# Performance work log

Measured on AMD Instinct MI355X. Metric: run time of the kernel, lower is better.

The kernel has to match this reference:

```python
import jax, jax.numpy as jnp
import numpy as np

N = 100000
E = 3200000
F_IN = 128
H = 64


def _glorot(key, fan_in, fan_out):
    lim = jnp.sqrt(6.0 / (fan_in + fan_out))
    return jax.random.uniform(key, (fan_in, fan_out), minval=-lim, maxval=lim, dtype=jnp.float32)


def setup_inputs() -> dict:
    key = jax.random.key(0)
    ks = jax.random.split(key, 16)
    x = jax.random.normal(ks[0], (N, F_IN), dtype=jnp.float32)
    edge_index = jax.random.randint(ks[1], (2, E), 0, N, dtype=jnp.int32)
    batch = jnp.zeros((N,), dtype=jnp.int32)
    dims = [(F_IN, H), (H, H // 2), (H // 2, H // 4), (H // 4, H // 2), (H // 2, H), (H, F_IN)]
    params = {}
    for i, (fi, fo) in enumerate(dims):
        params[f"W{i+1}"] = _glorot(ks[2 + i], fi, fo)
        params[f"b{i+1}"] = jnp.zeros((fo,), dtype=jnp.float32)
    params["Wf"] = _glorot(ks[10], F_IN, F_IN)
    params["bf"] = jnp.zeros((F_IN,), dtype=jnp.float32)
    return {"x": x, "edge_index": edge_index, "batch": batch, **params}


def _gcn_norm(edge_index, num_nodes):
    # PyG GCNConv: add self-loops, sym-normalize with deg^{-1/2}
    loop = jnp.arange(num_nodes, dtype=edge_index.dtype)
    row = jnp.concatenate([edge_index[0], loop])  # source j
    col = jnp.concatenate([edge_index[1], loop])  # target i
    deg = jax.ops.segment_sum(jnp.ones_like(col, dtype=jnp.float32), col, num_segments=num_nodes)
    dinv = jnp.where(deg > 0, jax.lax.rsqrt(deg), 0.0)
    norm = dinv[row] * dinv[col]
    return row, col, norm


def _gcn_conv(h, W, b, row, col, norm, num_nodes):
    h = h @ W  # linear first (no bias in lin), then normalized scatter-add
    msg = h[row] * norm[:, None]
    agg = jax.ops.segment_sum(msg, col, num_segments=num_nodes)
    return agg + b


def reference(x, edge_index, batch, W1, b1, W2, b2, W3, b3, W4, b4, W5, b5, W6, b6, Wf, bf):
    n = x.shape[0]
    row, col, norm = _gcn_norm(edge_index, n)
    h = jax.nn.relu(_gcn_conv(x, W1, b1, row, col, norm, n))
    h = jax.nn.relu(_gcn_conv(h, W2, b2, row, col, norm, n))
    h = jax.nn.relu(_gcn_conv(h, W3, b3, row, col, norm, n))
    h = jax.nn.relu(_gcn_conv(h, W4, b4, row, col, norm, n))
    h = jax.nn.relu(_gcn_conv(h, W5, b5, row, col, norm, n))
    h = jax.nn.relu(_gcn_conv(h, W6, b6, row, col, norm, n))
    return h @ Wf + bf
```

## Files before the change

### kernel.cpp

```cpp
#include <hip/hip_runtime.h>
#include <hip/hip_fp16.h>

#define BLK 256
#define NBSHIFT 9
#define MAXNB 200
#define GPART 512

typedef _Float16 half4v __attribute__((ext_vector_type(4)));
typedef _Float16 half8v __attribute__((ext_vector_type(8)));
typedef float    f32x4v __attribute__((ext_vector_type(4)));

__device__ __forceinline__ float4 ld4(const float* p) { return *(const float4*)p; }

__global__ __launch_bounds__(BLK) void p1_hist_k(const int* __restrict__ cols, int* __restrict__ hist,
                                                 int E, int nb) {
    __shared__ int h[MAXNB];
    const int tid = threadIdx.x, g = blockIdx.x;
    for (int b = tid; b < nb; b += BLK) h[b] = 0;
    __syncthreads();
    const int chunk = (E + GPART - 1) / GPART;
    const int start = g * chunk, end = min(E, start + chunk);
    for (int e = start + tid; e < end; e += BLK) atomicAdd(&h[cols[e] >> NBSHIFT], 1);
    __syncthreads();
    for (int b = tid; b < nb; b += BLK) hist[b * GPART + g] = h[b];
}
__global__ __launch_bounds__(256) void p2a_k(const int* __restrict__ hist, int* __restrict__ bstart,
                                             int nb, int E) {
    __shared__ int s[256];
    const int t = threadIdx.x;
    int tot = 0;
    if (t < nb) {
        const int* hp = &hist[t * GPART];
        for (int g = 0; g < GPART; g++) tot += hp[g];
    }
    s[t] = tot;
    __syncthreads();
    for (int o = 1; o < 256; o <<= 1) {
        int v = s[t] + ((t >= o) ? s[t - o] : 0);
        __syncthreads();
        s[t] = v;
        __syncthreads();
    }
    if (t < nb) bstart[t] = s[t] - tot;
    if (t == 0) bstart[nb] = E;
}
__global__ __launch_bounds__(256) void p2b_k(int* __restrict__ hist, const int* __restrict__ bstart) {
    __shared__ int s[GPART];
    const int b = blockIdx.x, t = threadIdx.x;
    const int v0 = hist[b * GPART + t], v1 = hist[b * GPART + 256 + t];
    s[t] = v0; s[256 + t] = v1;
    __syncthreads();
    for (int o = 1; o < GPART; o <<= 1) {
        const int a0 = s[t] + ((t >= o) ? s[t - o] : 0);
        const int a1 = s[256 + t] + ((256 + t >= o) ? s[256 + t - o] : 0);
        __syncthreads();
        s[t] = a0; s[256 + t] = a1;
        __syncthreads();
    }
    const int base = bstart[b];
    hist[b * GPART + t] = base + s[t] - v0;
    hist[b * GPART + 256 + t] = base + s[256 + t] - v1;
}
__global__ __launch_bounds__(BLK) void p3_part_k(const int* __restrict__ rows, const int* __restrict__ cols,
                                                 const int* __restrict__ hist, int2* __restrict__ pairs,
                                                 int E, int nb) {
    __shared__ int tail[MAXNB];
    const int tid = threadIdx.x, g = blockIdx.x;
    for (int b = tid; b < nb; b += BLK) tail[b] = hist[b * GPART + g];
    __syncthreads();
    const int chunk = (E + GPART - 1) / GPART;
    const int start = g * chunk, end = min(E, start + chunk);
    for (int e = start + tid; e < end; e += BLK) {
        const int r = rows[e], c = cols[e];
        const int pos = atomicAdd(&tail[c >> NBSHIFT], 1);
        pairs[pos] = make_int2(r, c);
    }
}
__global__ __launch_bounds__(BLK) void p4_fill_k(const int2* __restrict__ pairs, const int* __restrict__ bstart,
                                                 int* __restrict__ P, float* __restrict__ dinv,
                                                 int* __restrict__ srow, int n) {
    __shared__ int dh[1 << NBSHIFT];
    __shared__ int tl[1 << NBSHIFT];
    const int b = blockIdx.x, t = threadIdx.x;
    const int base = b << NBSHIFT;
    const int nnod = min(1 << NBSHIFT, n - base);
    const int lo = bstart[b], hi = bstart[b + 1];
    dh[t] = 0; dh[256 + t] = 0;
    __syncthreads();
    for (int e = lo + t; e < hi; e += BLK) atomicAdd(&dh[pairs[e].y - base], 1);
    __syncthreads();
    const int v0 = dh[t], v1 = dh[256 + t];
    tl[t] = v0; tl[256 + t] = v1;
    __syncthreads();
    for (int o = 1; o < (1 << NBSHIFT); o <<= 1) {
        const int a0 = tl[t] + ((t >= o) ? tl[t - o] : 0);
        const int a1 = tl[256 + t] + ((256 + t >= o) ? tl[256 + t - o] : 0);
        __syncthreads();
        tl[t] = a0; tl[256 + t] = a1;
        __syncthreads();
    }
    const int s0 = lo + tl[t] - v0;
    const int s1 = lo + tl[256 + t] - v1;
    __syncthreads();
    tl[t] = s0; tl[256 + t] = s1;
    if (t < nnod)       { P[base + t] = s0;       dinv[base + t] = rsqrtf((float)v0 + 1.0f); }
    if (256 + t < nnod) { P[base + 256 + t] = s1; dinv[base + 256 + t] = rsqrtf((float)v1 + 1.0f); }
    __syncthreads();
    for (int e = lo + t; e < hi; e += BLK) {
        const int2 pr = pairs[e];
        const int pos = atomicAdd(&tl[pr.y - base], 1);
        srow[pos] = pr.x;
    }
}

__device__ __forceinline__ void addh(float2 A[4], const __half* p) {
    const float4 raw = ld4((const float*)p);
    const __half2* h = (const __half2*)&raw;
    const float2 f0 = __half22float2(h[0]);
    const float2 f1 = __half22float2(h[1]);
    const float2 f2 = __half22float2(h[2]);
    const float2 f3 = __half22float2(h[3]);
    A[0].x += f0.x; A[0].y += f0.y;
    A[1].x += f1.x; A[1].y += f1.y;
    A[2].x += f2.x; A[2].y += f2.y;
    A[3].x += f3.x; A[3].y += f3.y;
}

template<int WD, bool PRE, bool OUTH>
__global__ __launch_bounds__(BLK) void gatherh_k(const __half* __restrict__ Tp, const int* __restrict__ P,
                                                 const int* __restrict__ srow, const float* __restrict__ dinv,
                                                 const float* __restrict__ bin, void* __restrict__ outv,
                                                 int n, int E) {
    constexpr int LPN = WD / 8;
    const long gid = (long)blockIdx.x * BLK + threadIdx.x;
    const int i = (int)(gid / LPN);
    if (i >= n) return;
    const int q = (int)(gid % LPN) * 8;
    const int start = P[i];
    const int end = (i + 1 < n) ? P[i + 1] : E;
    const float d = dinv[i];
    const __half* __restrict__ Tq = Tp + q;
    float2 A0[4], A1[4], A2[4], A3[4];
    {
        const float4 raw = ld4((const float*)(Tq + (long)i * WD));
        const __half2* h = (const __half2*)&raw;
        A0[0] = __half22float2(h[0]); A0[1] = __half22float2(h[1]);
        A0[2] = __half22float2(h[2]); A0[3] = __half22float2(h[3]);
    }
#pragma unroll
    for (int k = 0; k < 4; k++) {
        A1[k] = make_float2(0.f, 0.f); A2[k] = make_float2(0.f, 0.f); A3[k] = make_float2(0.f, 0.f);
    }
    int e = start;
    const int ea = min(end, (start + 3) & ~3);
    for (; e < ea; e++) addh(A0, Tq + (long)srow[e] * WD);
    for (; e + 8 <= end; e += 8) {
        const int4 j0 = *(const int4*)&srow[e];
        const int4 j1 = *(const int4*)&srow[e + 4];
        addh(A0, Tq + (long)j0.x * WD); addh(A1, Tq + (long)j0.y * WD);
        addh(A2, Tq + (long)j0.z * WD); addh(A3, Tq + (long)j0.w * WD);
        addh(A0, Tq + (long)j1.x * WD); addh(A1, Tq + (long)j1.y * WD);
        addh(A2, Tq + (long)j1.z * WD); addh(A3, Tq + (long)j1.w * WD);
    }
    if (e + 4 <= end) {
        const int4 j0 = *(const int4*)&srow[e];
        addh(A0, Tq + (long)j0.x * WD); addh(A1, Tq + (long)j0.y * WD);
        addh(A2, Tq + (long)j0.z * WD); addh(A3, Tq + (long)j0.w * WD);
        e += 4;
    }
    for (; e < end; e++) addh(A0, Tq + (long)srow[e] * WD);
#pragma unroll
    for (int k = 0; k < 4; k++) {
        A0[k].x += A1[k].x + A2[k].x + A3[k].x;
        A0[k].y += A1[k].y + A2[k].y + A3[k].y;
    }
    float v[8];
    v[0] = d * A0[0].x; v[1] = d * A0[0].y; v[2] = d * A0[1].x; v[3] = d * A0[1].y;
    v[4] = d * A0[2].x; v[5] = d * A0[2].y; v[6] = d * A0[3].x; v[7] = d * A0[3].y;
    if (PRE) {
        const float4 b0 = ld4(&bin[q]);
        const float4 b1 = ld4(&bin[q + 4]);
        v[0] = fmaxf(v[0] + b0.x, 0.f) * d; v[1] = fmaxf(v[1] + b0.y, 0.f) * d;
        v[2] = fmaxf(v[2] + b0.z, 0.f) * d; v[3] = fmaxf(v[3] + b0.w, 0.f) * d;
        v[4] = fmaxf(v[4] + b1.x, 0.f) * d; v[5] = fmaxf(v[5] + b1.y, 0.f) * d;
        v[6] = fmaxf(v[6] + b1.z, 0.f) * d; v[7] = fmaxf(v[7] + b1.w, 0.f) * d;
    }
    if (OUTH) {
        const __half2 h0 = __floats2half2_rn(v[0], v[1]);
        const __half2 h1 = __floats2half2_rn(v[2], v[3]);
        const __half2 h2 = __floats2half2_rn(v[4], v[5]);
        const __half2 h3 = __floats2half2_rn(v[6], v[7]);
        uint4 u;
        u.x = *(const unsigned int*)&h0; u.y = *(const unsigned int*)&h1;
        u.z = *(const unsigned int*)&h2; u.w = *(const unsigned int*)&h3;
        *(uint4*)((__half*)outv + (long)i * WD + q) = u;
    } else {
        float* out = (float*)outv;
        float4 v0, v1;
        v0.x = v[0]; v0.y = v[1]; v0.z = v[2]; v0.w = v[3];
        v1.x = v[4]; v1.y = v[5]; v1.z = v[6]; v1.w = v[7];
        *(float4*)&out[(long)i * WD + q] = v0;
        *(float4*)&out[(long)i * WD + q + 4] = v1;
    }
}

template<int FI, int FO, bool INB, bool OUTB, bool OUTRELU, bool OSC, bool OUTH>
__global__ __launch_bounds__(BLK) void gemm_k(const float* __restrict__ H, const float* __restrict__ Wm,
                                              const float* __restrict__ bin, const float* __restrict__ bout,
                                              const float* __restrict__ dinv, float* __restrict__ out, int n) {
    constexpr int COLT = FO / 4;
    constexpr int RTH  = BLK / COLT;
    constexpr int RPT  = (FO >= 64) ? 8 : 4;
    constexpr int ROWS = RTH * RPT;
    constexpr int KC   = (FI > 64) ? 64 : FI;
    constexpr int NKB  = FI / KC;

    __shared__ float Wl[KC * FO];
    __shared__ float Hl[ROWS * (KC + 1)];

    const int tid    = threadIdx.x;
    const int colIdx = tid % COLT;
    const int rowIdx = tid / COLT;
    const long rowBase = (long)blockIdx.x * ROWS;

    float4 acc[RPT];
#pragma unroll
    for (int i = 0; i < RPT; i++) acc[i] = make_float4(0.f, 0.f, 0.f, 0.f);

    for (int kb = 0; kb < NKB; kb++) {
        if (kb) __syncthreads();
        for (int f = tid * 4; f < KC * FO; f += BLK * 4) {
            const int kr = f / FO, c = f % FO;
            *(float4*)&Wl[kr * FO + c] = ld4(&Wm[(kb * KC + kr) * FO + c]);
        }
        for (int f = tid * 4; f < ROWS * KC; f += BLK * 4) {
            const int rr = f / KC, kk = f % KC;
            const long r = rowBase + rr;
            float4 v = make_float4(0.f, 0.f, 0.f, 0.f);
            if (r < n) v = ld4(&H[r * FI + kb * KC + kk]);
            if (INB) {
                float4 b4 = ld4(&bin[kb * KC + kk]);
                v.x = fmaxf(v.x + b4.x, 0.f); v.y = fmaxf(v.y + b4.y, 0.f);
                v.z = fmaxf(v.z + b4.z, 0.f); v.w = fmaxf(v.w + b4.w, 0.f);
            }
            float* dst = &Hl[rr * (KC + 1) + kk];
            dst[0] = v.x; dst[1] = v.y; dst[2] = v.z; dst[3] = v.w;
        }
        __syncthreads();
#pragma unroll 8
        for (int k = 0; k < KC; k++) {
            const float4 w4 = *(const float4*)&Wl[k * FO + 4 * colIdx];
#pragma unroll
            for (int i = 0; i < RPT; i++) {
                const float hv = Hl[(rowIdx * RPT + i) * (KC + 1) + k];
                acc[i].x = fmaf(hv, w4.x, acc[i].x);
                acc[i].y = fmaf(hv, w4.y, acc[i].y);
                acc[i].z = fmaf(hv, w4.z, acc[i].z);
                acc[i].w = fmaf(hv, w4.w, acc[i].w);
            }
        }
    }

    float4 bo = make_float4(0.f, 0.f, 0.f, 0.f);
    if (OUTB) bo = ld4(&bout[4 * colIdx]);
#pragma unroll
    for (int i = 0; i < RPT; i++) {
        const long r = rowBase + rowIdx * RPT + i;
        if (r < n) {
            float4 v = acc[i];
            if (OUTB) { v.x += bo.x; v.y += bo.y; v.z += bo.z; v.w += bo.w; }
            if (OUTRELU) {
                v.x = fmaxf(v.x, 0.f); v.y = fmaxf(v.y, 0.f);
                v.z = fmaxf(v.z, 0.f); v.w = fmaxf(v.w, 0.f);
            }
            if (OSC) {
                const float d = dinv[r];
                v.x *= d; v.y *= d; v.z *= d; v.w *= d;
            }
            if (OUTH) {
                const __half2 h01 = __floats2half2_rn(v.x, v.y);
                const __half2 h23 = __floats2half2_rn(v.z, v.w);
                uint2 u;
                u.x = *(const unsigned int*)&h01;
                u.y = *(const unsigned int*)&h23;
                *(uint2*)((__half*)out + r * FO + 4 * colIdx) = u;
            } else {
                *(float4*)&out[r * FO + 4 * colIdx] = v;
            }
        }
    }
}

template<int K, int FO, bool AH, bool OUTB, bool OUTRELU, bool OSC, bool OUTH>
__global__ __launch_bounds__(BLK) void mgemm_k(const void* __restrict__ Hv, const float* __restrict__ Wm,
                                               const float* __restrict__ bout, const float* __restrict__ dinv,
                                               void* __restrict__ outv, int n) {
    constexpr int BM = 128;
    constexpr int KP = K + 8;
    constexpr int NT = FO / 16;
    __shared__ _Float16 Al[BM * KP];
    __shared__ _Float16 Bl[FO * KP];

    const int tid = threadIdx.x;
    const long rowBase = (long)blockIdx.x * BM;

    for (int f = tid * 4; f < K * FO; f += BLK * 4) {
        const int nn = f / K, k0 = f % K;
        const int blk = k0 & ~31, g = (k0 >> 2) & 3, h = (k0 >> 4) & 1;
        half4v w4;
#pragma unroll
        for (int c = 0; c < 4; c++) w4[c] = (_Float16)Wm[(k0 + c) * FO + nn];
        *(half4v*)&Bl[nn * KP + blk + 8 * g + 4 * h] = w4;
    }
    if (AH) {
        const __half* Hp = (const __half*)Hv;
        for (int f = tid * 8; f < BM * K; f += BLK * 8) {
            const int rr = f / K, k0 = f % K;
            const long r = rowBase + rr;
            uint4 u = make_uint4(0u, 0u, 0u, 0u);
            if (r < n) u = *(const uint4*)&Hp[r * K + k0];
            const int blk = k0 & ~31, g0 = (k0 >> 2) & 3, h = (k0 >> 4) & 1;
            *(uint2*)&Al[rr * KP + blk + 8 * g0 + 4 * h] = make_uint2(u.x, u.y);
            *(uint2*)&Al[rr * KP + blk + 8 * (g0 + 1) + 4 * h] = make_uint2(u.z, u.w);
        }
    } else {
        const float* Hp = (const float*)Hv;
        for (int f = tid * 4; f < BM * K; f += BLK * 4) {
            const int rr = f / K, k0 = f % K;
            const long r = rowBase + rr;
            float4 v = make_float4(0.f, 0.f, 0.f, 0.f);
            if (r < n) v = ld4(&Hp[r * K + k0]);
            const int blk = k0 & ~31, g = (k0 >> 2) & 3, h = (k0 >> 4) & 1;
            half4v a4;
            a4[0] = (_Float16)v.x; a4[1] = (_Float16)v.y; a4[2] = (_Float16)v.z; a4[3] = (_Float16)v.w;
            *(half4v*)&Al[rr * KP + blk + 8 * g + 4 * h] = a4;
        }
    }
    __syncthreads();

    const int wv = tid >> 6;
    const int lane = tid & 63;
    const int lr = lane & 15;
    const int lg = lane >> 4;
    const int wrow = wv * 32;

    const f32x4v vzero = {0.f, 0.f, 0.f, 0.f};
    f32x4v acc[2][NT];
#pragma unroll
    for (int a = 0; a < 2; a++)
#pragma unroll
        for (int t = 0; t < NT; t++) acc[a][t] = vzero;

#pragma unroll
    for (int ks = 0; ks < K / 32; ks++) {
        const int ko = ks * 32 + 8 * lg;
        const half8v a0 = *(const half8v*)&Al[(wrow + lr) * KP + ko];
        const half8v a1 = *(const half8v*)&Al[(wrow + 16 + lr) * KP + ko];
#pragma unroll
        for (int nt = 0; nt < NT; nt++) {
            const half8v b = *(const half8v*)&Bl[(nt * 16 + lr) * KP + ko];
            acc[0][nt] = __builtin_amdgcn_mfma_f32_16x16x32_f16(a0, b, acc[0][nt], 0, 0, 0);
            acc[1][nt] = __builtin_amdgcn_mfma_f32_16x16x32_f16(a1, b, acc[1][nt], 0, 0, 0);
        }
    }

    float bo[NT];
    if (OUTB) {
#pragma unroll
        for (int nt = 0; nt < NT; nt++) bo[nt] = bout[nt * 16 + lr];
    }
#pragma unroll
    for (int rt = 0; rt < 2; rt++) {
#pragma unroll
        for (int r = 0; r < 4; r++) {
            const long row = rowBase + wrow + rt * 16 + lg * 4 + r;
            if (row < n) {
                const float d = OSC ? dinv[row] : 1.0f;
#pragma unroll
                for (int nt = 0; nt < NT; nt++) {
                    float v = acc[rt][nt][r];
                    if (OUTB) v += bo[nt];
                    if (OUTRELU) v = fmaxf(v, 0.f);
                    if (OSC) v *= d;
                    if (OUTH) ((__half*)outv)[row * FO + nt * 16 + lr] = __float2half_rn(v);
                    else      ((float*)outv)[row * FO + nt * 16 + lr] = v;
                }
            }
        }
    }
}

extern "C" void kernel_launch(void* const* d_in, const int* in_sizes, int n_in,
                              void* d_out, int out_size, void* d_ws, size_t ws_size,
                              hipStream_t stream)
{
    const float* x  = (const float*)d_in[0];
    const int*   ei = (const int*)d_in[1];
    const float* W1 = (const float*)d_in[3];  const float* b1 = (const float*)d_in[4];
    const float* W2 = (const float*)d_in[5];  const float* b2 = (const float*)d_in[6];
    const float* W3 = (const float*)d_in[7];  const float* b3 = (const float*)d_in[8];
    const float* W4 = (const float*)d_in[9];  const float* b4 = (const float*)d_in[10];
    const float* W5 = (const float*)d_in[11]; const float* b5 = (const float*)d_in[12];
    const float* W6 = (const float*)d_in[13]; const float* b6 = (const float*)d_in[14];
    const float* Wf = (const float*)d_in[15]; const float* bf = (const float*)d_in[16];

    const int n = in_sizes[0] / 128;
    const int E = in_sizes[1] / 2;
    const int* rows = ei;
    const int* cols = ei + E;

    int*   P    = (int*)d_ws;
    int*   srow = P + n;
    float* dinv = (float*)(srow + E);
    float* bufA = dinv + n;
    float* bufB = bufA + (size_t)n * 128;
    int2*  pairs = (int2*)bufA;
    int*   hist  = (int*)bufB;
    int*   bstart= hist + MAXNB * GPART;

    auto cdiv = [](long a, long b) { return (unsigned)((a + b - 1) / b); };
    const int nb = (n + (1 << NBSHIFT) - 1) >> NBSHIFT;

    p1_hist_k<<<GPART, BLK, 0, stream>>>(cols, hist, E, nb);
    p2a_k<<<1, 256, 0, stream>>>(hist, bstart, nb, E);
    p2b_k<<<nb, 256, 0, stream>>>(hist, bstart);
    p3_part_k<<<GPART, BLK, 0, stream>>>(rows, cols, hist, pairs, E, nb);
    p4_fill_k<<<nb, BLK, 0, stream>>>(pairs, bstart, P, dinv, srow, n);

    mgemm_k<128, 64, false, false, false, true, true><<<cdiv(n, 128), BLK, 0, stream>>>(x, W1, nullptr, dinv, bufA, n);
    gatherh_k<64, false, false><<<cdiv((long)n * 8, BLK), BLK, 0, stream>>>((const __half*)bufA, P, srow, dinv, nullptr, bufB, n, E);

    gemm_k<64, 32, true, false, false, true, true><<<cdiv(n, 128), BLK, 0, stream>>>(bufB, W2, b1, nullptr, dinv, bufA, n);
    gatherh_k<32, false, false><<<cdiv((long)n * 4, BLK), BLK, 0, stream>>>((const __half*)bufA, P, srow, dinv, nullptr, bufB, n, E);

    gemm_k<32, 16, true, false, false, true, true><<<cdiv(n, 256), BLK, 0, stream>>>(bufB, W3, b2, nullptr, dinv, bufA, n);
    gatherh_k<16, true, true><<<cdiv((long)n * 2, BLK), BLK, 0, stream>>>((const __half*)bufA, P, srow, dinv, b3, bufB, n, E);

    gatherh_k<16, false, false><<<cdiv((long)n * 2, BLK), BLK, 0, stream>>>((const __half*)bufB, P, srow, dinv, nullptr, bufA, n, E);
    gemm_k<16, 32, false, true, true, true, true><<<cdiv(n, 128), BLK, 0, stream>>>(bufA, W4, nullptr, b4, dinv, bufB, n);

    gatherh_k<32, false, false><<<cdiv((long)n * 4, BLK), BLK, 0, stream>>>((const __half*)bufB, P, srow, dinv, nullptr, bufA, n, E);
    gemm_k<32, 64, false, true, true, true, true><<<cdiv(n, 128), BLK, 0, stream>>>(bufA, W5, nullptr, b5, dinv, bufB, n);

    gatherh_k<64, false, true><<<cdiv((long)n * 8, BLK), BLK, 0, stream>>>((const __half*)bufB, P, srow, dinv, nullptr, bufA, n, E);
    mgemm_k<64, 128, true, true, true, false, true><<<cdiv(n, 128), BLK, 0, stream>>>(bufA, W6, b6, nullptr, bufB, n);

    mgemm_k<128, 128, true, true, false, false, false><<<cdiv(n, 128), BLK, 0, stream>>>(bufB, Wf, bf, nullptr, d_out, n);
}
```

Baseline: 664.7 us.

## Gather wide GCN layers in 16-column slices for cache locality

The GEMMs feeding wide aggregations now write their fp16 output as column slices of 16 halves per node (n*16 contiguous per slice). The aggregation then runs as one gather kernel per slice, writing into the interleaved output. Each slice covers only 3.2 MB, so random neighbour reads are meant to stay in L2/MALL instead of thrashing across the full feature table. The cost is more kernel launches and re-reading the CSR indices once per slice.

```diff
diff --git a/kernel.cpp b/kernel.cpp
--- a/kernel.cpp
+++ b/kernel.cpp
@@ -124,6 +124,74 @@
     A[1].x += f1.x; A[1].y += f1.y;
     A[2].x += f2.x; A[2].y += f2.y;
     A[3].x += f3.x; A[3].y += f3.y;
+}
+
+template<bool OUTH>
+__global__ __launch_bounds__(BLK) void gslice_k(const __half* __restrict__ Ts, const int* __restrict__ P,
+                                                const int* __restrict__ srow, const float* __restrict__ dinv,
+                                                void* __restrict__ outv, int n, int E, int qout, int WDO) {
+    const long gid = (long)blockIdx.x * BLK + threadIdx.x;
+    const int i = (int)(gid >> 1);
+    if (i >= n) return;
+    const int q = (int)(gid & 1) * 8;
+    const int start = P[i];
+    const int end = (i + 1 < n) ? P[i + 1] : E;
+    const float d = dinv[i];
+    const __half* __restrict__ Tq = Ts + q;
+    float2 A0[4], A1[4], A2[4], A3[4];
+    {
+        const float4 raw = ld4((const float*)(Tq + (long)i * 16));
+        const __half2* h = (const __half2*)&raw;
+        A0[0] = __half22float2(h[0]); A0[1] = __half22float2(h[1]);
+        A0[2] = __half22float2(h[2]); A0[3] = __half22float2(h[3]);
+    }
+#pragma unroll
+    for (int k = 0; k < 4; k++) {
+        A1[k] = make_float2(0.f, 0.f); A2[k] = make_float2(0.f, 0.f); A3[k] = make_float2(0.f, 0.f);
+    }
+    int e = start;
+    const int ea = min(end, (start + 3) & ~3);
+    for (; e < ea; e++) addh(A0, Tq + (long)srow[e] * 16);
+    for (; e + 8 <= end; e += 8) {
+        const int4 j0 = *(const int4*)&srow[e];
+        const int4 j1 = *(const int4*)&srow[e + 4];
+        addh(A0, Tq + (long)j0.x * 16); addh(A1, Tq + (long)j0.y * 16);
+        addh(A2, Tq + (long)j0.z * 16); addh(A3, Tq + (long)j0.w * 16);
+        addh(A0, Tq + (long)j1.x * 16); addh(A1, Tq + (long)j1.y * 16);
+        addh(A2, Tq + (long)j1.z * 16); addh(A3, Tq + (long)j1.w * 16);
+    }
+    if (e + 4 <= end) {
+        const int4 j0 = *(const int4*)&srow[e];
+        addh(A0, Tq + (long)j0.x * 16); addh(A1, Tq + (long)j0.y * 16);
+        addh(A2, Tq + (long)j0.z * 16); addh(A3, Tq + (long)j0.w * 16);
+        e += 4;
+    }
+    for (; e < end; e++) addh(A0, Tq + (long)srow[e] * 16);
+#pragma unroll
+    for (int k = 0; k < 4; k++) {
+        A0[k].x += A1[k].x + A2[k].x + A3[k].x;
+        A0[k].y += A1[k].y + A2[k].y + A3[k].y;
+    }
+    float v[8];
+    v[0] = d * A0[0].x; v[1] = d * A0[0].y; v[2] = d * A0[1].x; v[3] = d * A0[1].y;
+    v[4] = d * A0[2].x; v[5] = d * A0[2].y; v[6] = d * A0[3].x; v[7] = d * A0[3].y;
+    if (OUTH) {
+        const __half2 h0 = __floats2half2_rn(v[0], v[1]);
+        const __half2 h1 = __floats2half2_rn(v[2], v[3]);
+        const __half2 h2 = __floats2half2_rn(v[4], v[5]);
+        const __half2 h3 = __floats2half2_rn(v[6], v[7]);
+        uint4 u;
+        u.x = *(const unsigned int*)&h0; u.y = *(const unsigned int*)&h1;
+        u.z = *(const unsigned int*)&h2; u.w = *(const unsigned int*)&h3;
+        *(uint4*)&((__half*)outv)[(long)i * WDO + qout + q] = u;
+    } else {
+        float* o = (float*)outv;
+        float4 v0, v1;
+        v0.x = v[0]; v0.y = v[1]; v0.z = v[2]; v0.w = v[3];
+        v1.x = v[4]; v1.y = v[5]; v1.z = v[6]; v1.w = v[7];
+        *(float4*)&o[(long)i * WDO + qout + q] = v0;
+        *(float4*)&o[(long)i * WDO + qout + q + 4] = v1;
+    }
 }
 
 template<int WD, bool PRE, bool OUTH>
@@ -204,7 +272,7 @@
     }
 }
 
-template<int FI, int FO, bool INB, bool OUTB, bool OUTRELU, bool OSC, bool OUTH>
+template<int FI, int FO, bool INB, bool OUTB, bool OUTRELU, bool OSC, bool OUTH, bool SLICEH>
 __global__ __launch_bounds__(BLK) void gemm_k(const float* __restrict__ H, const float* __restrict__ Wm,
                                               const float* __restrict__ bin, const float* __restrict__ bout,
                                               const float* __restrict__ dinv, float* __restrict__ out, int n) {
@@ -283,7 +351,10 @@
                 uint2 u;
                 u.x = *(const unsigned int*)&h01;
                 u.y = *(const unsigned int*)&h23;
-                *(uint2*)((__half*)out + r * FO + 4 * colIdx) = u;
+                long base;
+                if (SLICEH) base = (long)(colIdx >> 2) * ((long)n * 16) + r * 16 + ((4 * colIdx) & 15);
+                else        base = r * FO + 4 * colIdx;
+                *(uint2*)((__half*)out + base) = u;
             } else {
                 *(float4*)&out[r * FO + 4 * colIdx] = v;
             }
@@ -291,7 +362,7 @@
     }
 }
 
-template<int K, int FO, bool AH, bool OUTB, bool OUTRELU, bool OSC, bool OUTH>
+template<int K, int FO, bool AH, bool OUTB, bool OUTRELU, bool OSC, bool OUTH, bool SLICE>
 __global__ __launch_bounds__(BLK) void mgemm_k(const void* __restrict__ Hv, const float* __restrict__ Wm,
                                                const float* __restrict__ bout, const float* __restrict__ dinv,
                                                void* __restrict__ outv, int n) {
@@ -382,8 +453,12 @@
                     if (OUTB) v += bo[nt];
                     if (OUTRELU) v = fmaxf(v, 0.f);
                     if (OSC) v *= d;
-                    if (OUTH) ((__half*)outv)[row * FO + nt * 16 + lr] = __float2half_rn(v);
-                    else      ((float*)outv)[row * FO + nt * 16 + lr] = v;
+                    if (OUTH) {
+                        if (SLICE) ((__half*)outv)[(long)nt * ((long)n * 16) + row * 16 + lr] = __float2half_rn(v);
+                        else       ((__half*)outv)[row * FO + nt * 16 + lr] = __float2half_rn(v);
+                    } else {
+                        ((float*)outv)[row * FO + nt * 16 + lr] = v;
+                    }
                 }
             }
         }
@@ -420,6 +495,7 @@
 
     auto cdiv = [](long a, long b) { return (unsigned)((a + b - 1) / b); };
     const int nb = (n + (1 << NBSHIFT) - 1) >> NBSHIFT;
+    const size_t SL = (size_t)n * 16;
 
     p1_hist_k<<<GPART, BLK, 0, stream>>>(cols, hist, E, nb);
     p2a_k<<<1, 256, 0, stream>>>(hist, bstart, nb, E);
@@ -427,23 +503,29 @@
     p3_part_k<<<GPART, BLK, 0, stream>>>(rows, cols, hist, pairs, E, nb);
     p4_fill_k<<<nb, BLK, 0, stream>>>(pairs, bstart, P, dinv, srow, n);
 
-    mgemm_k<128, 64, false, false, false, true, true><<<cdiv(n, 128), BLK, 0, stream>>>(x, W1, nullptr, dinv, bufA, n);
-    gatherh_k<64, false, false><<<cdiv((long)n * 8, BLK), BLK, 0, stream>>>((const __half*)bufA, P, srow, dinv, nullptr, bufB, n, E);
-
-    gemm_k<64, 32, true, false, false, true, true><<<cdiv(n, 128), BLK, 0, stream>>>(bufB, W2, b1, nullptr, dinv, bufA, n);
-    gatherh_k<32, false, false><<<cdiv((long)n * 4, BLK), BLK, 0, stream>>>((const __half*)bufA, P, srow, dinv, nullptr, bufB, n, E);
-
-    gemm_k<32, 16, true, false, false, true, true><<<cdiv(n, 256), BLK, 0, stream>>>(bufB, W3, b2, nullptr, dinv, bufA, n);
+    const unsigned GG = cdiv((long)n * 2, BLK);
+
+    mgemm_k<128, 64, false, false, false, true, true, true><<<cdiv(n, 128), BLK, 0, stream>>>(x, W1, nullptr, dinv, bufA, n);
+    for (int s = 0; s < 4; s++)
+        gslice_k<false><<<GG, BLK, 0, stream>>>((const __half*)bufA + s * SL, P, srow, dinv, bufB, n, E, s * 16, 64);
+
+    gemm_k<64, 32, true, false, false, true, true, true><<<cdiv(n, 128), BLK, 0, stream>>>(bufB, W2, b1, nullptr, dinv, bufA, n);
+    for (int s = 0; s < 2; s++)
+        gslice_k<false><<<GG, BLK, 0, stream>>>((const __half*)bufA + s * SL, P, srow, dinv, bufB, n, E, s * 16, 32);
+
+    gemm_k<32, 16, true, false, false, true, true, false><<<cdiv(n, 256), BLK, 0, stream>>>(bufB, W3, b2, nullptr, dinv, bufA, n);
     gatherh_k<16, true, true><<<cdiv((long)n * 2, BLK), BLK, 0, stream>>>((const __half*)bufA, P, srow, dinv, b3, bufB, n, E);
 
     gatherh_k<16, false, false><<<cdiv((long)n * 2, BLK), BLK, 0, stream>>>((const __half*)bufB, P, srow, dinv, nullptr, bufA, n, E);
-    gemm_k<16, 32, false, true, true, true, true><<<cdiv(n, 128), BLK, 0, stream>>>(bufA, W4, nullptr, b4, dinv, bufB, n);
-
-    gatherh_k<32, false, false><<<cdiv((long)n * 4, BLK), BLK, 0, stream>>>((const __half*)bufB, P, srow, dinv, nullptr, bufA, n, E);
-    gemm_k<32, 64, false, true, true, true, true><<<cdiv(n, 128), BLK, 0, stream>>>(bufA, W5, nullptr, b5, dinv, bufB, n);
-
-    gatherh_k<64, false, true><<<cdiv((long)n * 8, BLK), BLK, 0, stream>>>((const __half*)bufB, P, srow, dinv, nullptr, bufA, n, E);
-    mgemm_k<64, 128, true, true, true, false, true><<<cdiv(n, 128), BLK, 0, stream>>>(bufA, W6, b6, nullptr, bufB, n);
-
-    mgemm_k<128, 128, true, true, false, false, false><<<cdiv(n, 128), BLK, 0, stream>>>(bufB, Wf, bf, nullptr, d_out, n);
-}
+    gemm_k<16, 32, false, true, true, true, true, true><<<cdiv(n, 128), BLK, 0, stream>>>(bufA, W4, nullptr, b4, dinv, bufB, n);
+
+    for (int s = 0; s < 2; s++)
+        gslice_k<false><<<GG, BLK, 0, stream>>>((const __half*)bufB + s * SL, P, srow, dinv, bufA, n, E, s * 16, 32);
+    gemm_k<32, 64, false, true, true, true, true, true><<<cdiv(n, 128), BLK, 0, stream>>>(bufA, W5, nullptr, b5, dinv, bufB, n);
+
+    for (int s = 0; s < 4; s++)
+        gslice_k<true><<<GG, BLK, 0, stream>>>((const __half*)bufB + s * SL, P, srow, dinv, bufA, n, E, s * 16, 64);
+    mgemm_k<64, 128, true, true, true, false, true, false><<<cdiv(n, 128), BLK, 0, stream>>>(bufA, W6, b6, nullptr, bufB, n);
+
+    mgemm_k<128, 128, true, true, false, false, false, false><<<cdiv(n, 128), BLK, 0, stream>>>(bufB, Wf, bf, nullptr, d_out, n);
+}
```

After: 827.0 us. 1.24x slower.
